# Kernel tuning notes

Measured on AMD Instinct MI355X. Metric: run time of the kernel, lower is better.

Reference implementation:

```python
import jax, jax.numpy as jnp
import numpy as np

B, T, C = 4, 2048, 1024
N_HEAD = 16


def setup_inputs() -> dict:
    key = jax.random.key(0)
    k1, k2, k3, k4, k5 = jax.random.split(key, 5)
    x = jax.random.normal(k1, (B, T, C), dtype=jnp.float32)
    # c_attn: Dense(3*C) -> kernel [C, 3C], bias [3C]
    w_attn = jax.random.normal(k2, (C, 3 * C), dtype=jnp.float32) * 0.02
    b_attn = jnp.zeros((3 * C,), dtype=jnp.float32)
    # c_proj: Dense(C) with scaled init 0.02/sqrt(2*n_layer), n_layer=24
    w_proj = jax.random.normal(k3, (C, C), dtype=jnp.float32) * (0.02 / np.sqrt(2 * 24))
    b_proj = jnp.zeros((C,), dtype=jnp.float32)
    return {"x": x, "w_attn": w_attn, "b_attn": b_attn, "w_proj": w_proj, "b_proj": b_proj}


def reference(x, w_attn, b_attn, w_proj, b_proj):
    Bx, Tx, Cx = x.shape
    hd = Cx // N_HEAD  # head dim
    qkv = x @ w_attn + b_attn                      # [B, T, 3C]
    q, k, v = jnp.split(qkv, 3, axis=2)
    q = q.reshape(Bx, Tx, N_HEAD, hd).transpose(0, 2, 1, 3)  # [B, H, T, hd]
    k = k.reshape(Bx, Tx, N_HEAD, hd).transpose(0, 2, 1, 3)
    v = v.reshape(Bx, Tx, N_HEAD, hd).transpose(0, 2, 1, 3)
    mask = jnp.tril(jnp.ones((1, 1, Tx, Tx), dtype=bool))
    att = jnp.einsum('bhqd,bhkd->bhqk', q, k) / jnp.sqrt(jnp.float32(hd))
    att = jnp.where(mask, att, jnp.finfo(jnp.float32).min)
    att = jax.nn.softmax(att, axis=-1)
    y = jnp.einsum('bhqk,bhkd->bhqd', att, v)      # [B, H, T, hd]
    y = y.transpose(0, 2, 1, 3).reshape(Bx, Tx, Cx)
    return y @ w_proj + b_proj
```

## Files before the change

kernel.cpp:

```cpp
#include <hip/hip_runtime.h>
#include <cstdint>
#include <cstddef>

typedef unsigned short u16;
typedef __bf16 bf16_t;
typedef bf16_t bf16x8 __attribute__((ext_vector_type(8)));
typedef float f32x4 __attribute__((ext_vector_type(4)));

__device__ __forceinline__ u16 f32_to_bf16(float f) {
  uint32_t u = __builtin_bit_cast(uint32_t, f);
  u += 0x7fffu + ((u >> 16) & 1u);
  return (u16)(u >> 16);
}

__device__ __forceinline__ uint32_t pack_bf16x2(float lo, float hi) {
  uint32_t a = __builtin_bit_cast(uint32_t, hi) + 0x8000u;
  uint32_t b = __builtin_bit_cast(uint32_t, lo) + 0x8000u;
  return __builtin_amdgcn_perm(a, b, 0x07060302u);
}

__device__ __forceinline__ void gload_lds16(const void* g, void* l) {
  __builtin_amdgcn_global_load_lds(
      (const __attribute__((address_space(1))) unsigned int*)g,
      (__attribute__((address_space(3))) unsigned int*)l, 16, 0, 0);
}

__global__ void cvt_bf16(const float* __restrict__ in, u16* __restrict__ out, int n) {
  int i = (blockIdx.x * 256 + threadIdx.x) * 4;
  if (i < n) {
    float4 f = *(const float4*)(in + i);
    ushort4 o;
    o.x = f32_to_bf16(f.x); o.y = f32_to_bf16(f.y);
    o.z = f32_to_bf16(f.z); o.w = f32_to_bf16(f.w);
    *(ushort4*)(out + i) = o;
  }
}

__global__ void tconv(const float* __restrict__ in, u16* __restrict__ out, int R, int C) {
  __shared__ u16 t[64][80];
  int tid = threadIdx.x;
  int cb = blockIdx.x * 64, rb = blockIdx.y * 64;
  int rr = tid >> 2, cg = (tid & 3) * 16;
  const float* ip = in + (size_t)(rb + rr) * C + cb + cg;
#pragma unroll
  for (int i = 0; i < 16; ++i) t[rr][cg + i] = f32_to_bf16(ip[i]);
  __syncthreads();
  int cc = tid >> 2, rg = (tid & 3) * 16;
  u16* op = out + (size_t)(cb + cc) * R + rb + rg;
  union { uint4 v[2]; u16 s[16]; } tmp;
#pragma unroll
  for (int i = 0; i < 16; ++i) tmp.s[i] = t[rg + i][cc];
  *(uint4*)op = tmp.v[0];
  *(uint4*)(op + 8) = tmp.v[1];
}

__global__ void vtrans(const u16* __restrict__ qkvb, u16* __restrict__ vt) {
  __shared__ u16 t[64][80];
  int tid = threadIdx.x;
  int bh = blockIdx.x, tb = blockIdx.y * 64;
  int b = bh >> 4, h = bh & 15;
  int tt = tid >> 2, dg = (tid & 3) * 16;
  const u16* ip = qkvb + (size_t)(b * 2048 + tb + tt) * 3072 + 2048 + h * 64 + dg;
  union { uint4 v; u16 s[8]; } a0, a1;
  a0.v = *(const uint4*)ip;
  a1.v = *(const uint4*)(ip + 8);
#pragma unroll
  for (int i = 0; i < 8; ++i) { t[tt][dg + i] = a0.s[i]; t[tt][dg + 8 + i] = a1.s[i]; }
  __syncthreads();
  int dd = tid >> 2, tg = (tid & 3) * 16;
  u16* op = vt + (size_t)(bh * 64 + dd) * 2048 + tb + tg;
  union { uint4 v[2]; u16 s[16]; } tmp;
#pragma unroll
  for (int i = 0; i < 16; ++i) tmp.s[i] = t[tg + i][dd];
  *(uint4*)op = tmp.v[0];
  *(uint4*)(op + 8) = tmp.v[1];
}

template <int OUT_BF16>
__global__ __launch_bounds__(512, 2) void gemm256(const u16* __restrict__ A,
                                                  const u16* __restrict__ Bt,
                                                  const float* __restrict__ bias,
                                                  void* __restrict__ Cout,
                                                  int M, int N, int K) {
  __shared__ __align__(16) u16 lds[2][2][16384];
  const int tid = threadIdx.x;
  const int w = tid >> 6, L = tid & 63;
  const int quad = L >> 4, lc = L & 15;
  const int wr = w >> 2, wc = w & 3;
  const int wrM = wr * 128, wcN = wc * 64;
  const int rL = L >> 3;
  const int gsw = (L & 7) ^ rL;

  const int nbx = N >> 8;
  const int cpx = gridDim.x >> 3;
  const int id = blockIdx.x;
  const int swz = (id & 7) * cpx + (id >> 3);
  const int tileN = (swz % nbx) << 8;
  const int tileM = (swz / nbx) << 8;
  const int nkt = K >> 6;

  u16* const A0 = &lds[0][0][0];
  u16* const B0 = &lds[0][1][0];
  u16* const A1 = &lds[1][0][0];
  u16* const B1 = &lds[1][1][0];

  auto stageQ = [&](const u16* Mp, int gRow, int kt, u16* reg) {
    int ktc = kt < nkt ? kt : nkt - 1;
    const u16* src = Mp + (size_t)(gRow + w * 8 + rL) * K + (ktc << 6) + gsw * 8;
    gload_lds16(src, reg + w * 512);
  };

  f32x4 acc[8][4] = {};
  const int rsw = lc & 7;
  const int g0 = (quad ^ rsw) * 8;
  const int g1 = ((4 + quad) ^ rsw) * 8;
  const int aRow = (wrM + lc) * 64;
  const int bRow = (wcN + lc) * 64;

  stageQ(A, tileM + 0, 0, A0 + 0);
  stageQ(A, tileM + 128, 0, A0 + 8192);
  stageQ(Bt, tileN + 0, 0, B0 + 0);
  stageQ(Bt, tileN + 64, 0, B0 + 4096);
  stageQ(A, tileM + 64, 0, A0 + 4096);
  stageQ(A, tileM + 192, 0, A0 + 12288);
  stageQ(Bt, tileN + 128, 0, B0 + 8192);
  stageQ(Bt, tileN + 192, 0, B0 + 12288);
  stageQ(A, tileM + 0, 1, A1 + 0);
  stageQ(A, tileM + 128, 1, A1 + 8192);
  stageQ(Bt, tileN + 0, 1, B1 + 0);
  stageQ(Bt, tileN + 64, 1, B1 + 4096);
  stageQ(A, tileM + 64, 1, A1 + 4096);
  stageQ(A, tileM + 192, 1, A1 + 12288);
  asm volatile("s_waitcnt vmcnt(6)" ::: "memory");
  __builtin_amdgcn_s_barrier();

  auto group = [&](u16* Ab, u16* Bb, u16* Bob, int T) {
    bf16x8 af[4][2], blo[2][2], bhi[2][2];
#pragma unroll
    for (int mi = 0; mi < 4; ++mi) {
      af[mi][0] = *(const bf16x8*)&Ab[aRow + mi * 1024 + g0];
      af[mi][1] = *(const bf16x8*)&Ab[aRow + mi * 1024 + g1];
    }
#pragma unroll
    for (int ni = 0; ni < 2; ++ni) {
      blo[ni][0] = *(const bf16x8*)&Bb[bRow + ni * 1024 + g0];
      blo[ni][1] = *(const bf16x8*)&Bb[bRow + ni * 1024 + g1];
    }
    stageQ(Bt, tileN + 128, T + 1, Bob + 8192);
    stageQ(Bt, tileN + 192, T + 1, Bob + 12288);
    asm volatile("" ::: "memory");
    __builtin_amdgcn_s_barrier();
    asm volatile("s_waitcnt lgkmcnt(0)" ::: "memory");
    __builtin_amdgcn_s_setprio(1);
#pragma unroll
    for (int mi = 0; mi < 4; ++mi)
#pragma unroll
      for (int ni = 0; ni < 2; ++ni) {
        acc[mi][ni] = __builtin_amdgcn_mfma_f32_16x16x32_bf16(af[mi][0], blo[ni][0], acc[mi][ni], 0, 0, 0);
        acc[mi][ni] = __builtin_amdgcn_mfma_f32_16x16x32_bf16(af[mi][1], blo[ni][1], acc[mi][ni], 0, 0, 0);
      }
    __builtin_amdgcn_s_setprio(0);
    asm volatile("" ::: "memory");
    __builtin_amdgcn_s_barrier();
#pragma unroll
    for (int ni = 0; ni < 2; ++ni) {
      bhi[ni][0] = *(const bf16x8*)&Bb[bRow + (2 + ni) * 1024 + g0];
      bhi[ni][1] = *(const bf16x8*)&Bb[bRow + (2 + ni) * 1024 + g1];
    }
    stageQ(A, tileM + 0, T + 2, Ab + 0);
    stageQ(A, tileM + 128, T + 2, Ab + 8192);
    asm volatile("" ::: "memory");
    __builtin_amdgcn_s_barrier();
    asm volatile("s_waitcnt lgkmcnt(0)" ::: "memory");
    __builtin_amdgcn_s_setprio(1);
#pragma unroll
    for (int mi = 0; mi < 4; ++mi)
#pragma unroll
      for (int ni = 0; ni < 2; ++ni) {
        acc[mi][ni + 2] = __builtin_amdgcn_mfma_f32_16x16x32_bf16(af[mi][0], bhi[ni][0], acc[mi][ni + 2], 0, 0, 0);
        acc[mi][ni + 2] = __builtin_amdgcn_mfma_f32_16x16x32_bf16(af[mi][1], bhi[ni][1], acc[mi][ni + 2], 0, 0, 0);
      }
    __builtin_amdgcn_s_setprio(0);
    asm volatile("" ::: "memory");
    __builtin_amdgcn_s_barrier();
#pragma unroll
    for (int mi = 0; mi < 4; ++mi) {
      af[mi][0] = *(const bf16x8*)&Ab[aRow + (4 + mi) * 1024 + g0];
      af[mi][1] = *(const bf16x8*)&Ab[aRow + (4 + mi) * 1024 + g1];
    }
    stageQ(Bt, tileN + 0, T + 2, Bb + 0);
    stageQ(Bt, tileN + 64, T + 2, Bb + 4096);
    asm volatile("" ::: "memory");
    __builtin_amdgcn_s_barrier();
    asm volatile("s_waitcnt lgkmcnt(0)" ::: "memory");
    __builtin_amdgcn_s_setprio(1);
#pragma unroll
    for (int mi = 0; mi < 4; ++mi)
#pragma unroll
      for (int ni = 0; ni < 2; ++ni) {
        acc[mi + 4][ni + 2] = __builtin_amdgcn_mfma_f32_16x16x32_bf16(af[mi][0], bhi[ni][0], acc[mi + 4][ni + 2], 0, 0, 0);
        acc[mi + 4][ni + 2] = __builtin_amdgcn_mfma_f32_16x16x32_bf16(af[mi][1], bhi[ni][1], acc[mi + 4][ni + 2], 0, 0, 0);
      }
    __builtin_amdgcn_s_setprio(0);
    asm volatile("" ::: "memory");
    __builtin_amdgcn_s_barrier();
    stageQ(A, tileM + 64, T + 2, Ab + 4096);
    stageQ(A, tileM + 192, T + 2, Ab + 12288);
    asm volatile("" ::: "memory");
    __builtin_amdgcn_s_barrier();
    __builtin_amdgcn_s_setprio(1);
#pragma unroll
    for (int mi = 0; mi < 4; ++mi)
#pragma unroll
      for (int ni = 0; ni < 2; ++ni) {
        acc[mi + 4][ni] = __builtin_amdgcn_mfma_f32_16x16x32_bf16(af[mi][0], blo[ni][0], acc[mi + 4][ni], 0, 0, 0);
        acc[mi + 4][ni] = __builtin_amdgcn_mfma_f32_16x16x32_bf16(af[mi][1], blo[ni][1], acc[mi + 4][ni], 0, 0, 0);
      }
    __builtin_amdgcn_s_setprio(0);
    asm volatile("s_waitcnt vmcnt(6)" ::: "memory");
    __builtin_amdgcn_s_barrier();
  };

  for (int T = 0; T < nkt; T += 2) {
    group(A0, B0, B1, T);
    group(A1, B1, B0, T + 1);
  }

  asm volatile("s_waitcnt vmcnt(0)" ::: "memory");

#pragma unroll
  for (int mi = 0; mi < 8; ++mi) {
    int rowb = tileM + wrM + mi * 16 + quad * 4;
#pragma unroll
    for (int ni = 0; ni < 4; ++ni) {
      int col = tileN + wcN + ni * 16 + lc;
      float bv = bias[col];
#pragma unroll
      for (int r = 0; r < 4; ++r) {
        float v = acc[mi][ni][r] + bv;
        if (OUT_BF16)
          ((u16*)Cout)[(size_t)(rowb + r) * N + col] = f32_to_bf16(v);
        else
          ((float*)Cout)[(size_t)(rowb + r) * N + col] = v;
      }
    }
  }
}

__global__ __launch_bounds__(256, 4) void attn(const u16* __restrict__ qkvb,
                                               const u16* __restrict__ vt,
                                               u16* __restrict__ yb) {
  __shared__ __align__(16) u16 kbuf[8 * 512];
  __shared__ __align__(16) u16 vbuf[8 * 512];
  __shared__ __align__(16) u16 pbuf[4][1024];
  const int tid = threadIdx.x;
  const int w = tid >> 6, L = tid & 63;
  const int quad = L >> 4, lc = L & 15;
  const int bh = blockIdx.x;
  const int b = bh >> 4, h = bh & 15;
  const int pair = blockIdx.y;
  const float e_c = 0.18033688f;
  u16* pb = (u16*)pbuf[w];

  for (int pass = 0; pass < 2; ++pass) {
    const int qt = pass ? (31 - pair) : pair;
    const int qbase = qt * 64;
    const int q_loc = w * 16 + lc;

    bf16x8 qf[2];
    {
      const u16* qp = qkvb + ((size_t)(b * 2048 + qbase + q_loc) * 3072 + h * 64 + quad * 8);
      qf[0] = *(const bf16x8*)qp;
      qf[1] = *(const bf16x8*)(qp + 32);
    }
    f32x4 o[4] = {};
    float lsum = 0.f;

    for (int kb = 0; kb <= qbase; kb += 64) {
      const bool diag = (kb == qbase);
      __syncthreads();
#pragma unroll
      for (int i = 0; i < 4; ++i) {
        int fb = w * 4 + i;
        if (fb < 8) {
          int nt = fb >> 1, ks = fb & 1;
          int tk = kb + nt * 16 + lc;
          int d = ks * 32 + quad * 8;
          gload_lds16(qkvb + ((size_t)(b * 2048 + tk) * 3072 + 1024 + h * 64 + d), &kbuf[fb * 512]);
        } else {
          int f = fb - 8;
          int dt = f >> 1, ks = f & 1;
          int d = dt * 16 + lc;
          int tk = kb + ks * 32 + quad * 8;
          gload_lds16(vt + ((size_t)(bh * 64 + d) * 2048 + tk), &vbuf[f * 512]);
        }
      }
      __syncthreads();

      f32x4 s[4];
#pragma unroll
      for (int nt = 0; nt < 4; ++nt) {
        s[nt] = (f32x4){0.f, 0.f, 0.f, 0.f};
#pragma unroll
        for (int ks = 0; ks < 2; ++ks) {
          bf16x8 kf = *(const bf16x8*)&kbuf[(nt * 2 + ks) * 512 + L * 8];
          s[nt] = __builtin_amdgcn_mfma_f32_16x16x32_bf16(kf, qf[ks], s[nt], 0, 0, 0);
        }
      }

#pragma unroll
      for (int nt = 0; nt < 4; ++nt) {
        float p0 = __builtin_amdgcn_exp2f(s[nt][0] * e_c);
        float p1 = __builtin_amdgcn_exp2f(s[nt][1] * e_c);
        float p2 = __builtin_amdgcn_exp2f(s[nt][2] * e_c);
        float p3 = __builtin_amdgcn_exp2f(s[nt][3] * e_c);
        if (diag) {
          int tk0 = nt * 16 + quad * 4;
          p0 = (tk0 + 0 > q_loc) ? 0.f : p0;
          p1 = (tk0 + 1 > q_loc) ? 0.f : p1;
          p2 = (tk0 + 2 > q_loc) ? 0.f : p2;
          p3 = (tk0 + 3 > q_loc) ? 0.f : p3;
        }
        lsum += (p0 + p1) + (p2 + p3);
        uint2 pk;
        pk.x = pack_bf16x2(p0, p1);
        pk.y = pack_bf16x2(p2, p3);
        int idx = (nt >> 1) * 512 + (((nt & 1) * 2 + (quad >> 1)) * 16 + lc) * 8 + (quad & 1) * 4;
        *(uint2*)&pb[idx] = pk;
      }

#pragma unroll
      for (int ks = 0; ks < 2; ++ks) {
        bf16x8 pf = *(const bf16x8*)&pb[ks * 512 + L * 8];
#pragma unroll
        for (int dt = 0; dt < 4; ++dt) {
          bf16x8 vf = *(const bf16x8*)&vbuf[(dt * 2 + ks) * 512 + L * 8];
          o[dt] = __builtin_amdgcn_mfma_f32_16x16x32_bf16(vf, pf, o[dt], 0, 0, 0);
        }
      }
    }

    lsum += __shfl_xor(lsum, 16);
    lsum += __shfl_xor(lsum, 32);
    float inv = 1.f / lsum;

    {
      u16* yp = yb + (size_t)(b * 2048 + qbase + q_loc) * 1024 + h * 64 + quad * 4;
#pragma unroll
      for (int dt = 0; dt < 4; ++dt) {
        uint2 pk;
        pk.x = pack_bf16x2(o[dt][0] * inv, o[dt][1] * inv);
        pk.y = pack_bf16x2(o[dt][2] * inv, o[dt][3] * inv);
        *(uint2*)(yp + dt * 16) = pk;
      }
    }
  }
}

extern "C" void kernel_launch(void* const* d_in, const int* in_sizes, int n_in,
                              void* d_out, int out_size, void* d_ws, size_t ws_size,
                              hipStream_t stream) {
  const float* x = (const float*)d_in[0];
  const float* w_attn = (const float*)d_in[1];
  const float* b_attn = (const float*)d_in[2];
  const float* w_proj = (const float*)d_in[3];
  const float* b_proj = (const float*)d_in[4];
  float* out = (float*)d_out;

  char* ws = (char*)d_ws;
  u16* xb = (u16*)ws;    ws += (size_t)8192 * 1024 * 2;
  u16* waT = (u16*)ws;   ws += (size_t)3072 * 1024 * 2;
  u16* wpT = (u16*)ws;   ws += (size_t)1024 * 1024 * 2;
  u16* qkvb = (u16*)ws;  ws += (size_t)8192 * 3072 * 2;
  u16* vtb = (u16*)ws;   ws += (size_t)64 * 64 * 2048 * 2;
  u16* yb = (u16*)ws;    ws += (size_t)8192 * 1024 * 2;

  cvt_bf16<<<8192, 256, 0, stream>>>(x, xb, 8192 * 1024);
  tconv<<<dim3(3072 / 64, 1024 / 64), 256, 0, stream>>>(w_attn, waT, 1024, 3072);
  tconv<<<dim3(1024 / 64, 1024 / 64), 256, 0, stream>>>(w_proj, wpT, 1024, 1024);
  gemm256<1><<<dim3(384), 512, 0, stream>>>(xb, waT, b_attn, qkvb, 8192, 3072, 1024);
  vtrans<<<dim3(64, 32), 256, 0, stream>>>(qkvb, vtb);
  attn<<<dim3(64, 16), 256, 0, stream>>>(qkvb, vtb, yb);
  gemm256<0><<<dim3(128), 512, 0, stream>>>(yb, wpT, b_proj, out, 8192, 1024, 1024);
}
```

Before: 268.9 us.

## Double-buffer K/V tiles in attention with prefetch and MFMA priority boosts

The attention kernel now keeps two LDS buffers for the K and V tiles. Each iteration issues the async global-to-LDS loads for the next key block while computing on the current one. This replaces the old load, barrier, compute sequence and drops one barrier per iteration. The end of each pass prefetches block 0 for the next pass, and s_setprio raises wave priority around the MFMA sections. The risk is that cross-wave visibility of the prefetched data relies on the compiler placing vmcnt waits; those waits may also serialize on the fresh prefetch, which would cancel the overlap. LDS use also rises.

```diff
diff --git a/kernel.cpp b/kernel.cpp
--- a/kernel.cpp
+++ b/kernel.cpp
@@ -250,8 +250,7 @@
 __global__ __launch_bounds__(256, 4) void attn(const u16* __restrict__ qkvb,
                                                const u16* __restrict__ vt,
                                                u16* __restrict__ yb) {
-  __shared__ __align__(16) u16 kbuf[8 * 512];
-  __shared__ __align__(16) u16 vbuf[8 * 512];
+  __shared__ __align__(16) u16 kv[2][16][512];
   __shared__ __align__(16) u16 pbuf[4][1024];
   const int tid = threadIdx.x;
   const int w = tid >> 6, L = tid & 63;
@@ -262,6 +261,24 @@
   const float e_c = 0.18033688f;
   u16* pb = (u16*)pbuf[w];
 
+  const bool isK = (w < 2);
+  const u16* sbase = isK
+      ? qkvb + ((size_t)(b * 2048 + w * 32 + lc) * 3072 + 1024 + h * 64 + quad * 8)
+      : vt + ((size_t)(bh * 64 + (w - 2) * 32 + lc) * 2048 + quad * 8);
+  const size_t fo1 = isK ? (size_t)16 * 3072 : (size_t)16 * 2048;
+
+  auto stage = [&](int nkb, int buf) {
+    const u16* s = sbase + (isK ? (size_t)nkb * 3072 : (size_t)nkb);
+    u16* d = &kv[buf][w * 4][0];
+    gload_lds16(s, d);
+    gload_lds16(s + 32, d + 512);
+    gload_lds16(s + fo1, d + 1024);
+    gload_lds16(s + fo1 + 32, d + 1536);
+  };
+
+  int par = 0;
+  stage(0, 0);
+
   for (int pass = 0; pass < 2; ++pass) {
     const int qt = pass ? (31 - pair) : pair;
     const int qbase = qt * 64;
@@ -279,34 +296,21 @@
     for (int kb = 0; kb <= qbase; kb += 64) {
       const bool diag = (kb == qbase);
       __syncthreads();
-#pragma unroll
-      for (int i = 0; i < 4; ++i) {
-        int fb = w * 4 + i;
-        if (fb < 8) {
-          int nt = fb >> 1, ks = fb & 1;
-          int tk = kb + nt * 16 + lc;
-          int d = ks * 32 + quad * 8;
-          gload_lds16(qkvb + ((size_t)(b * 2048 + tk) * 3072 + 1024 + h * 64 + d), &kbuf[fb * 512]);
-        } else {
-          int f = fb - 8;
-          int dt = f >> 1, ks = f & 1;
-          int d = dt * 16 + lc;
-          int tk = kb + ks * 32 + quad * 8;
-          gload_lds16(vt + ((size_t)(bh * 64 + d) * 2048 + tk), &vbuf[f * 512]);
-        }
-      }
-      __syncthreads();
+      const int nkb = (kb < qbase) ? kb + 64 : 0;
+      stage(nkb, par ^ 1);
 
       f32x4 s[4];
+      __builtin_amdgcn_s_setprio(1);
 #pragma unroll
       for (int nt = 0; nt < 4; ++nt) {
         s[nt] = (f32x4){0.f, 0.f, 0.f, 0.f};
 #pragma unroll
         for (int ks = 0; ks < 2; ++ks) {
-          bf16x8 kf = *(const bf16x8*)&kbuf[(nt * 2 + ks) * 512 + L * 8];
+          bf16x8 kf = *(const bf16x8*)&kv[par][nt * 2 + ks][L * 8];
           s[nt] = __builtin_amdgcn_mfma_f32_16x16x32_bf16(kf, qf[ks], s[nt], 0, 0, 0);
         }
       }
+      __builtin_amdgcn_s_setprio(0);
 
 #pragma unroll
       for (int nt = 0; nt < 4; ++nt) {
@@ -329,15 +333,19 @@
         *(uint2*)&pb[idx] = pk;
       }
 
+      __builtin_amdgcn_s_setprio(1);
 #pragma unroll
       for (int ks = 0; ks < 2; ++ks) {
         bf16x8 pf = *(const bf16x8*)&pb[ks * 512 + L * 8];
 #pragma unroll
         for (int dt = 0; dt < 4; ++dt) {
-          bf16x8 vf = *(const bf16x8*)&vbuf[(dt * 2 + ks) * 512 + L * 8];
+          bf16x8 vf = *(const bf16x8*)&kv[par][8 + dt * 2 + ks][L * 8];
           o[dt] = __builtin_amdgcn_mfma_f32_16x16x32_bf16(vf, pf, o[dt], 0, 0, 0);
         }
       }
+      __builtin_amdgcn_s_setprio(0);
+
+      par ^= 1;
     }
 
     lsum += __shfl_xor(lsum, 16);
@@ -355,6 +363,8 @@
       }
     }
   }
+
+  asm volatile("s_waitcnt vmcnt(0)" ::: "memory");
 }
 
 extern "C" void kernel_launch(void* const* d_in, const int* in_sizes, int n_in,
```

Result: no change. 272.4 us (+1.3%).
